# Kernel optimization log

Hardware: AMD Instinct MI355X
Metric: run time of the kernel (lower is better)

The kernel has to match this reference:

```python
import jax, jax.numpy as jnp
import numpy as np

D = 1024      # feat_dim
H = 16        # n_heads
HD = D // H   # head_dim
G = 32        # number of image/text groups
P = 128       # patch tokens per image
T = 32        # text tokens per caption
SUM_P = G * P # 4096
BT = G * T    # 1024


def setup_inputs() -> dict:
    key = jax.random.key(0)
    ks = jax.random.split(key, 16)
    s = (6.0 / (2 * D)) ** 0.5  # xavier_uniform bound
    def xavier(k):
        return jax.random.uniform(k, (D, D), jnp.float32, -s, s)
    return {
        "V_token": jax.random.normal(ks[0], (SUM_P, D), jnp.float32),
        "L_token": jax.random.normal(ks[1], (BT, D), jnp.float32),
        "image_split_list": jnp.full((G,), P, dtype=jnp.int32),
        "text_split_list": jnp.full((G,), T, dtype=jnp.int32),
        "Wq_w": xavier(ks[2]), "Wq_b": jnp.zeros((D,), jnp.float32),
        "Wk_w": xavier(ks[3]), "Wk_b": jnp.zeros((D,), jnp.float32),
        "Wv_w": xavier(ks[4]), "Wv_b": jnp.zeros((D,), jnp.float32),
        "Wo_w": xavier(ks[5]), "Wo_b": jnp.zeros((D,), jnp.float32),
        "Wm_w": xavier(ks[6]), "Wm_b": jnp.zeros((D,), jnp.float32),
        "Wv2_w": xavier(ks[7]), "Wv2_b": jnp.zeros((D,), jnp.float32),
    }


def reference(V_token, L_token, image_split_list, text_split_list,
              Wq_w, Wq_b, Wk_w, Wk_b, Wv_w, Wv_b,
              Wo_w, Wo_b, Wm_w, Wm_b, Wv2_w, Wv2_b):
    sum_p, bt = V_token.shape[0], L_token.shape[0]
    g = image_split_list.shape[0]
    # segment ids (equivalent to torch.cat of torch.full per group)
    v_seg = jnp.repeat(jnp.arange(g), image_split_list, total_repeat_length=sum_p)
    l_seg = jnp.repeat(jnp.arange(g), text_split_list, total_repeat_length=bt)
    mask = v_seg[:, None] != l_seg[None, :]  # [sum_p, bt], True = masked out

    Q = (V_token @ Wq_w.T + Wq_b).reshape(sum_p, H, HD)
    K = (L_token @ Wk_w.T + Wk_b).reshape(bt, H, HD)
    Vl = (L_token @ Wv_w.T + Wv_b).reshape(bt, H, HD)

    scores = jnp.einsum('phd,thd->hpt', Q, K) / (HD ** 0.5)  # [H, sum_p, bt]
    scores = jnp.where(mask[None, :, :], -jnp.inf, scores)
    attn = jax.nn.softmax(scores, axis=-1)
    ctx = jnp.einsum('hpt,thd->phd', attn, Vl).reshape(sum_p, D)

    out = ctx @ Wo_w.T + Wo_b
    mu = out @ Wm_w.T + Wm_b
    log_var = out @ Wv2_w.T + Wv2_b
    return mu, log_var, attn
```

## Files before the change

### kernel.cpp

```cpp
#include <hip/hip_runtime.h>
#include <hip/hip_fp16.h>

#define K_DIM 1024

typedef _Float16 f16x8 __attribute__((ext_vector_type(8)));
typedef _Float16 f16x4 __attribute__((ext_vector_type(4)));
typedef float f32x4_t __attribute__((ext_vector_type(4)));

__global__ __launch_bounds__(256) void cvt_f32_to_f16(const float* __restrict__ in,
                                                      _Float16* __restrict__ out, int n4) {
  int stride = gridDim.x * blockDim.x;
  for (int i = blockIdx.x * blockDim.x + threadIdx.x; i < n4; i += stride) {
    float4 v = reinterpret_cast<const float4*>(in)[i];
    f16x4 h;
    h[0] = (_Float16)v.x; h[1] = (_Float16)v.y; h[2] = (_Float16)v.z; h[3] = (_Float16)v.w;
    reinterpret_cast<f16x4*>(out)[i] = h;
  }
}

template <bool OUTH>
__global__ __launch_bounds__(256) void gemm_nt(
    const _Float16* __restrict__ A,
    const _Float16* __restrict__ Wa, const _Float16* __restrict__ Wb,
    const float* __restrict__ ba, const float* __restrict__ bb,
    void* __restrict__ Ca, void* __restrict__ Cb) {
  const _Float16* __restrict__ W = (blockIdx.z == 0) ? Wa : Wb;
  const float* __restrict__ bias = (blockIdx.z == 0) ? ba : bb;
  void* __restrict__ Cv = (blockIdx.z == 0) ? Ca : Cb;

  __shared__ _Float16 Ash[128][40];
  __shared__ _Float16 Bsh[128][40];

  const int tid = threadIdx.x;
  const int lane = tid & 63;
  const int wave = tid >> 6;
  const int wr = wave >> 1;
  const int wc = wave & 1;

  const int tm = blockIdx.x * 128;
  const int tn = blockIdx.y * 128;

  const int r0 = tid >> 2;
  const int kk0 = (tid & 3) * 8;

  const _Float16* Ag0 = A + (size_t)(tm + r0) * K_DIM + kk0;
  const _Float16* Ag1 = A + (size_t)(tm + r0 + 64) * K_DIM + kk0;
  const _Float16* Bg0 = W + (size_t)(tn + r0) * K_DIM + kk0;
  const _Float16* Bg1 = W + (size_t)(tn + r0 + 64) * K_DIM + kk0;

  f32x4_t acc[4][4];
#pragma unroll
  for (int m = 0; m < 4; ++m)
#pragma unroll
    for (int n = 0; n < 4; ++n) acc[m][n] = (f32x4_t){0.f, 0.f, 0.f, 0.f};

  uint4 pa0 = *(const uint4*)(Ag0);
  uint4 pa1 = *(const uint4*)(Ag1);
  uint4 pb0 = *(const uint4*)(Bg0);
  uint4 pb1 = *(const uint4*)(Bg1);

  const int fr = lane & 15;
  const int kc = (lane >> 4) * 8;

#pragma unroll 1
  for (int kt = 0; kt < K_DIM / 32; ++kt) {
    __syncthreads();
    *(uint4*)&Ash[r0][kk0] = pa0;
    *(uint4*)&Ash[r0 + 64][kk0] = pa1;
    *(uint4*)&Bsh[r0][kk0] = pb0;
    *(uint4*)&Bsh[r0 + 64][kk0] = pb1;
    __syncthreads();
    if (kt + 1 < K_DIM / 32) {
      const int koff = (kt + 1) * 32;
      pa0 = *(const uint4*)(Ag0 + koff);
      pa1 = *(const uint4*)(Ag1 + koff);
      pb0 = *(const uint4*)(Bg0 + koff);
      pb1 = *(const uint4*)(Bg1 + koff);
    }
    f16x8 af[4], bf[4];
#pragma unroll
    for (int m = 0; m < 4; ++m) af[m] = *(const f16x8*)&Ash[wr * 64 + m * 16 + fr][kc];
#pragma unroll
    for (int n = 0; n < 4; ++n) bf[n] = *(const f16x8*)&Bsh[wc * 64 + n * 16 + fr][kc];
#pragma unroll
    for (int m = 0; m < 4; ++m)
#pragma unroll
      for (int n = 0; n < 4; ++n)
        acc[m][n] = __builtin_amdgcn_mfma_f32_16x16x32_f16(af[m], bf[n], acc[m][n], 0, 0, 0);
  }

  const int cr = (lane >> 4) * 4;
  const int cc = lane & 15;
#pragma unroll
  for (int m = 0; m < 4; ++m) {
#pragma unroll
    for (int n = 0; n < 4; ++n) {
      const int col = tn + wc * 64 + n * 16 + cc;
      const float bv = bias[col];
#pragma unroll
      for (int r = 0; r < 4; ++r) {
        const int row = tm + wr * 64 + m * 16 + cr + r;
        float v = acc[m][n][r] + bv;
        if (OUTH)
          ((_Float16*)Cv)[(size_t)row * 1024 + col] = (_Float16)v;
        else
          ((float*)Cv)[(size_t)row * 1024 + col] = v;
      }
    }
  }
}

__global__ __launch_bounds__(256) void attn_kernel(
    const float* __restrict__ Q, const float* __restrict__ Kf, const float* __restrict__ Vf,
    float* __restrict__ attn_out,
    _Float16* __restrict__ ctx) {
  const int g = blockIdx.x;
  const int h = blockIdx.y;

  __shared__ float Ksh[32][68];
  __shared__ float Vsh[32][68];
  __shared__ float Arow[128][33];

  const int tid = threadIdx.x;

#pragma unroll
  for (int i = 0; i < 8; ++i) {
    int idx = tid + i * 256;
    int t = idx >> 6, d = idx & 63;
    Ksh[t][d] = Kf[(size_t)(g * 32 + t) * 1024 + h * 64 + d];
    Vsh[t][d] = Vf[(size_t)(g * 32 + t) * 1024 + h * 64 + d];
  }
  __syncthreads();

  const int p = tid >> 1;
  const int half = tid & 1;

  float4 qv[16];
  const float* qrow = Q + (size_t)(g * 128 + p) * 1024 + h * 64;
#pragma unroll
  for (int i = 0; i < 16; ++i) qv[i] = ((const float4*)qrow)[i];

  float s[16];
#pragma unroll
  for (int j = 0; j < 16; ++j) {
    int t = half * 16 + j;
    float acc = 0.f;
#pragma unroll
    for (int d4 = 0; d4 < 16; ++d4) {
      float4 kv = *(const float4*)&Ksh[t][d4 * 4];
      acc += qv[d4].x * kv.x + qv[d4].y * kv.y + qv[d4].z * kv.z + qv[d4].w * kv.w;
    }
    s[j] = acc * 0.125f;
  }

  float m = s[0];
#pragma unroll
  for (int j = 1; j < 16; ++j) m = fmaxf(m, s[j]);
  m = fmaxf(m, __shfl_xor(m, 1));
  float e[16];
  float sum = 0.f;
#pragma unroll
  for (int j = 0; j < 16; ++j) {
    e[j] = __expf(s[j] - m);
    sum += e[j];
  }
  sum += __shfl_xor(sum, 1);
  const float inv = 1.0f / sum;

  float* arow_out =
      attn_out + (size_t)h * 4096 * 1024 + (size_t)(g * 128 + p) * 1024 + g * 32 + half * 16;
#pragma unroll
  for (int j = 0; j < 16; ++j) {
    float a = e[j] * inv;
    arow_out[j] = a;
    Arow[p][half * 16 + j] = a;
  }
  __syncthreads();

  float4 acc4[8];
#pragma unroll
  for (int i = 0; i < 8; ++i) acc4[i] = (float4){0.f, 0.f, 0.f, 0.f};
#pragma unroll
  for (int t = 0; t < 32; ++t) {
    float av = Arow[p][t];
#pragma unroll
    for (int d4 = 0; d4 < 8; ++d4) {
      float4 v = *(const float4*)&Vsh[t][half * 32 + d4 * 4];
      acc4[d4].x += av * v.x;
      acc4[d4].y += av * v.y;
      acc4[d4].z += av * v.z;
      acc4[d4].w += av * v.w;
    }
  }
  _Float16* crow = ctx + (size_t)(g * 128 + p) * 1024 + h * 64 + half * 32;
#pragma unroll
  for (int i = 0; i < 4; ++i) {
    f16x8 hv;
    float4 lo = acc4[i * 2], hi = acc4[i * 2 + 1];
    hv[0] = (_Float16)lo.x; hv[1] = (_Float16)lo.y;
    hv[2] = (_Float16)lo.z; hv[3] = (_Float16)lo.w;
    hv[4] = (_Float16)hi.x; hv[5] = (_Float16)hi.y;
    hv[6] = (_Float16)hi.z; hv[7] = (_Float16)hi.w;
    *(f16x8*)&crow[i * 8] = hv;
  }
}

extern "C" void kernel_launch(void* const* d_in, const int* in_sizes, int n_in,
                              void* d_out, int out_size, void* d_ws, size_t ws_size,
                              hipStream_t stream) {
  const float* V_token = (const float*)d_in[0];
  const float* L_token = (const float*)d_in[1];
  const float* Wq_w = (const float*)d_in[4];
  const float* Wq_b = (const float*)d_in[5];
  const float* Wk_w = (const float*)d_in[6];
  const float* Wk_b = (const float*)d_in[7];
  const float* Wv_w = (const float*)d_in[8];
  const float* Wv_b = (const float*)d_in[9];
  const float* Wo_w = (const float*)d_in[10];
  const float* Wo_b = (const float*)d_in[11];
  const float* Wm_w = (const float*)d_in[12];
  const float* Wm_b = (const float*)d_in[13];
  const float* Wv2_w = (const float*)d_in[14];
  const float* Wv2_b = (const float*)d_in[15];

  char* ws = (char*)d_ws;
  _Float16* hV = (_Float16*)ws;  ws += (size_t)4096 * 1024 * 2;
  _Float16* hL = (_Float16*)ws;  ws += (size_t)1024 * 1024 * 2;
  _Float16* hWq = (_Float16*)ws; ws += (size_t)1024 * 1024 * 2;
  _Float16* hWk = (_Float16*)ws; ws += (size_t)1024 * 1024 * 2;
  _Float16* hWv = (_Float16*)ws; ws += (size_t)1024 * 1024 * 2;
  _Float16* hWo = (_Float16*)ws; ws += (size_t)1024 * 1024 * 2;
  _Float16* hWm = (_Float16*)ws; ws += (size_t)1024 * 1024 * 2;
  _Float16* hWv2 = (_Float16*)ws; ws += (size_t)1024 * 1024 * 2;
  float* Qf = (float*)ws;        ws += (size_t)4096 * 1024 * 4;
  float* Kf = (float*)ws;        ws += (size_t)1024 * 1024 * 4;
  float* Vf = (float*)ws;        ws += (size_t)1024 * 1024 * 4;
  _Float16* ctx = (_Float16*)ws; ws += (size_t)4096 * 1024 * 2;
  _Float16* outh = (_Float16*)ws; ws += (size_t)4096 * 1024 * 2;

  float* mu = (float*)d_out;
  float* logv = mu + (size_t)4096 * 1024;
  float* attn = mu + (size_t)2 * 4096 * 1024;

  hipMemsetAsync(attn, 0, (size_t)16 * 4096 * 1024 * 4, stream);

  auto cvt = [&](const float* in, _Float16* out, size_t n) {
    int n4 = (int)(n / 4);
    int blocks = (n4 + 255) / 256;
    if (blocks > 2048) blocks = 2048;
    hipLaunchKernelGGL(cvt_f32_to_f16, dim3(blocks), dim3(256), 0, stream, in, out, n4);
  };
  cvt(V_token, hV, (size_t)4096 * 1024);
  cvt(L_token, hL, (size_t)1024 * 1024);
  cvt(Wq_w, hWq, (size_t)1024 * 1024);
  cvt(Wk_w, hWk, (size_t)1024 * 1024);
  cvt(Wv_w, hWv, (size_t)1024 * 1024);
  cvt(Wo_w, hWo, (size_t)1024 * 1024);
  cvt(Wm_w, hWm, (size_t)1024 * 1024);
  cvt(Wv2_w, hWv2, (size_t)1024 * 1024);

  hipLaunchKernelGGL((gemm_nt<false>), dim3(32, 8, 1), dim3(256), 0, stream,
                     hV, hWq, hWq, Wq_b, Wq_b, (void*)Qf, (void*)Qf);
  hipLaunchKernelGGL((gemm_nt<false>), dim3(8, 8, 2), dim3(256), 0, stream,
                     hL, hWk, hWv, Wk_b, Wv_b, (void*)Kf, (void*)Vf);
  hipLaunchKernelGGL(attn_kernel, dim3(32, 16), dim3(256), 0, stream, Qf, Kf, Vf, attn, ctx);
  hipLaunchKernelGGL((gemm_nt<true>), dim3(32, 8, 1), dim3(256), 0, stream,
                     ctx, hWo, hWo, Wo_b, Wo_b, (void*)outh, (void*)outh);
  hipLaunchKernelGGL((gemm_nt<false>), dim3(32, 8, 2), dim3(256), 0, stream,
                     outh, hWm, hWv2, Wm_b, Wv2_b, (void*)mu, (void*)logv);
}
```

Measured before the change: 176.8 us.

## Fuse attn zero-fill into GEMM launches and shrink GEMM tiles to 128x64

Drops the standalone memset of the large attention output and splits the zero-fill across two GEMM kernels as extra z-slices. Heads 0-7 are zeroed alongside the QKV projection. Off-diagonal blocks of heads 8-15 are zeroed alongside the mu/logvar projection, skipping the blocks the attention kernel writes. It also batches the eight fp32-to-fp16 conversions into one launch, merges the Q/K/V GEMMs into one launch, and halves the GEMM N-tile to 64 for more blocks. The intent is to overlap the memory-bound fill with compute and cut launch count, at the cost of less reuse per GEMM tile and uneven block workloads.

```diff
diff --git a/kernel.cpp b/kernel.cpp
--- a/kernel.cpp
+++ b/kernel.cpp
@@ -1,35 +1,37 @@
 #include <hip/hip_runtime.h>
 #include <hip/hip_fp16.h>
-
-#define K_DIM 1024
 
 typedef _Float16 f16x8 __attribute__((ext_vector_type(8)));
 typedef _Float16 f16x4 __attribute__((ext_vector_type(4)));
 typedef float f32x4_t __attribute__((ext_vector_type(4)));
 
-__global__ __launch_bounds__(256) void cvt_f32_to_f16(const float* __restrict__ in,
-                                                      _Float16* __restrict__ out, int n4) {
-  int stride = gridDim.x * blockDim.x;
+struct CvtArgs {
+  const float* src[8];
+  _Float16* dst[8];
+  int n4[8];
+};
+
+__global__ __launch_bounds__(256) void cvt_all(CvtArgs a) {
+  const int t = blockIdx.y;
+  const float4* __restrict__ in = (const float4*)a.src[t];
+  f16x4* __restrict__ out = (f16x4*)a.dst[t];
+  const int n4 = a.n4[t];
+  const int stride = gridDim.x * blockDim.x;
   for (int i = blockIdx.x * blockDim.x + threadIdx.x; i < n4; i += stride) {
-    float4 v = reinterpret_cast<const float4*>(in)[i];
+    float4 v = in[i];
     f16x4 h;
     h[0] = (_Float16)v.x; h[1] = (_Float16)v.y; h[2] = (_Float16)v.z; h[3] = (_Float16)v.w;
-    reinterpret_cast<f16x4*>(out)[i] = h;
+    out[i] = h;
   }
 }
 
 template <bool OUTH>
-__global__ __launch_bounds__(256) void gemm_nt(
-    const _Float16* __restrict__ A,
-    const _Float16* __restrict__ Wa, const _Float16* __restrict__ Wb,
-    const float* __restrict__ ba, const float* __restrict__ bb,
-    void* __restrict__ Ca, void* __restrict__ Cb) {
-  const _Float16* __restrict__ W = (blockIdx.z == 0) ? Wa : Wb;
-  const float* __restrict__ bias = (blockIdx.z == 0) ? ba : bb;
-  void* __restrict__ Cv = (blockIdx.z == 0) ? Ca : Cb;
-
+__device__ __forceinline__ void gemm_tile(const _Float16* __restrict__ A,
+                                          const _Float16* __restrict__ W,
+                                          const float* __restrict__ bias,
+                                          void* __restrict__ Cv, int tm, int tn) {
   __shared__ _Float16 Ash[128][40];
-  __shared__ _Float16 Bsh[128][40];
+  __shared__ _Float16 Bsh[64][40];
 
   const int tid = threadIdx.x;
   const int lane = tid & 63;
@@ -37,55 +39,49 @@
   const int wr = wave >> 1;
   const int wc = wave & 1;
 
-  const int tm = blockIdx.x * 128;
-  const int tn = blockIdx.y * 128;
-
-  const int r0 = tid >> 2;
-  const int kk0 = (tid & 3) * 8;
-
-  const _Float16* Ag0 = A + (size_t)(tm + r0) * K_DIM + kk0;
-  const _Float16* Ag1 = A + (size_t)(tm + r0 + 64) * K_DIM + kk0;
-  const _Float16* Bg0 = W + (size_t)(tn + r0) * K_DIM + kk0;
-  const _Float16* Bg1 = W + (size_t)(tn + r0 + 64) * K_DIM + kk0;
-
-  f32x4_t acc[4][4];
+  const int ar = tid >> 1;
+  const int ac = (tid & 1) * 16;
+  const int br = tid >> 2;
+  const int bc = (tid & 3) * 8;
+
+  const _Float16* Ag = A + (size_t)(tm + ar) * 1024 + ac;
+  const _Float16* Bg = W + (size_t)(tn + br) * 1024 + bc;
+
+  f32x4_t acc[4][2];
 #pragma unroll
   for (int m = 0; m < 4; ++m)
 #pragma unroll
-    for (int n = 0; n < 4; ++n) acc[m][n] = (f32x4_t){0.f, 0.f, 0.f, 0.f};
-
-  uint4 pa0 = *(const uint4*)(Ag0);
-  uint4 pa1 = *(const uint4*)(Ag1);
-  uint4 pb0 = *(const uint4*)(Bg0);
-  uint4 pb1 = *(const uint4*)(Bg1);
+    for (int n = 0; n < 2; ++n) acc[m][n] = (f32x4_t){0.f, 0.f, 0.f, 0.f};
+
+  uint4 pa0 = *(const uint4*)(Ag);
+  uint4 pa1 = *(const uint4*)(Ag + 8);
+  uint4 pb = *(const uint4*)(Bg);
 
   const int fr = lane & 15;
   const int kc = (lane >> 4) * 8;
 
 #pragma unroll 1
-  for (int kt = 0; kt < K_DIM / 32; ++kt) {
+  for (int kt = 0; kt < 32; ++kt) {
     __syncthreads();
-    *(uint4*)&Ash[r0][kk0] = pa0;
-    *(uint4*)&Ash[r0 + 64][kk0] = pa1;
-    *(uint4*)&Bsh[r0][kk0] = pb0;
-    *(uint4*)&Bsh[r0 + 64][kk0] = pb1;
+    *(uint4*)&Ash[ar][ac] = pa0;
+    *(uint4*)&Ash[ar][ac + 8] = pa1;
+    *(uint4*)&Bsh[br][bc] = pb;
     __syncthreads();
-    if (kt + 1 < K_DIM / 32) {
-      const int koff = (kt + 1) * 32;
-      pa0 = *(const uint4*)(Ag0 + koff);
-      pa1 = *(const uint4*)(Ag1 + koff);
-      pb0 = *(const uint4*)(Bg0 + koff);
-      pb1 = *(const uint4*)(Bg1 + koff);
-    }
-    f16x8 af[4], bf[4];
+    if (kt + 1 < 32) {
+      const int ko = (kt + 1) * 32;
+      pa0 = *(const uint4*)(Ag + ko);
+      pa1 = *(const uint4*)(Ag + ko + 8);
+      pb = *(const uint4*)(Bg + ko);
+    }
+    f16x8 af[4], bf[2];
 #pragma unroll
     for (int m = 0; m < 4; ++m) af[m] = *(const f16x8*)&Ash[wr * 64 + m * 16 + fr][kc];
 #pragma unroll
-    for (int n = 0; n < 4; ++n) bf[n] = *(const f16x8*)&Bsh[wc * 64 + n * 16 + fr][kc];
+    for (int n = 0; n < 2; ++n) bf[n] = *(const f16x8*)&Bsh[wc * 32 + n * 16 + fr][kc];
 #pragma unroll
     for (int m = 0; m < 4; ++m)
 #pragma unroll
-      for (int n = 0; n < 4; ++n)
+      for (int n = 0; n < 2; ++n)
         acc[m][n] = __builtin_amdgcn_mfma_f32_16x16x32_f16(af[m], bf[n], acc[m][n], 0, 0, 0);
   }
 
@@ -94,8 +90,8 @@
 #pragma unroll
   for (int m = 0; m < 4; ++m) {
 #pragma unroll
-    for (int n = 0; n < 4; ++n) {
-      const int col = tn + wc * 64 + n * 16 + cc;
+    for (int n = 0; n < 2; ++n) {
+      const int col = tn + wc * 32 + n * 16 + cc;
       const float bv = bias[col];
 #pragma unroll
       for (int r = 0; r < 4; ++r) {
@@ -108,6 +104,67 @@
       }
     }
   }
+}
+
+__global__ __launch_bounds__(256) void gemm_qkv_fill(
+    const _Float16* __restrict__ hV, const _Float16* __restrict__ hL,
+    const _Float16* __restrict__ hWq, const _Float16* __restrict__ hWk,
+    const _Float16* __restrict__ hWv,
+    const float* __restrict__ bq, const float* __restrict__ bk, const float* __restrict__ bv,
+    float* __restrict__ Qf, float* __restrict__ Kf, float* __restrict__ Vf,
+    float* __restrict__ attn) {
+  const int z = blockIdx.z;
+  if (z == 3) {
+    const int bl = blockIdx.y * 32 + blockIdx.x;
+    float4* base = (float4*)attn + (size_t)bl * 16384;
+    const float4 z4 = {0.f, 0.f, 0.f, 0.f};
+#pragma unroll
+    for (int c = threadIdx.x; c < 16384; c += 256) base[c] = z4;
+    return;
+  }
+  if (z != 0 && blockIdx.x >= 8) return;
+
+  const _Float16* A = (z == 0) ? hV : hL;
+  const _Float16* W = (z == 0) ? hWq : (z == 1) ? hWk : hWv;
+  const float* bias = (z == 0) ? bq : (z == 1) ? bk : bv;
+  float* C = (z == 0) ? Qf : (z == 1) ? Kf : Vf;
+  gemm_tile<false>(A, W, bias, (void*)C, blockIdx.x * 128, blockIdx.y * 64);
+}
+
+__global__ __launch_bounds__(256) void gemm_wo(
+    const _Float16* __restrict__ ctx, const _Float16* __restrict__ hWo,
+    const float* __restrict__ bo, _Float16* __restrict__ outh) {
+  gemm_tile<true>(ctx, hWo, bo, (void*)outh, blockIdx.x * 128, blockIdx.y * 64);
+}
+
+__global__ __launch_bounds__(256) void gemm_mv_fill(
+    const _Float16* __restrict__ outh,
+    const _Float16* __restrict__ hWm, const _Float16* __restrict__ hWv2,
+    const float* __restrict__ bm, const float* __restrict__ bv2,
+    float* __restrict__ mu, float* __restrict__ logv, float* __restrict__ attn) {
+  const int z = blockIdx.z;
+  if (z == 2) {
+    const int bl = blockIdx.y * 32 + blockIdx.x;
+    const int wave = threadIdx.x >> 6;
+    const int lane = threadIdx.x & 63;
+    const float4 z4 = {0.f, 0.f, 0.f, 0.f};
+#pragma unroll
+    for (int i = 0; i < 16; ++i) {
+      const int rowIdx = bl * 64 + i * 4 + wave;
+      const int p = rowIdx & 4095;
+      const int g8 = (p >> 7) * 8;
+      float4* row = (float4*)(attn + ((size_t)(8 + (rowIdx >> 12)) * 4096 + p) * 1024);
+#pragma unroll
+      for (int c = lane; c < 256; c += 64) {
+        if (c < g8 || c >= g8 + 8) row[c] = z4;
+      }
+    }
+    return;
+  }
+  const _Float16* W = z ? hWv2 : hWm;
+  const float* bias = z ? bv2 : bm;
+  float* C = z ? logv : mu;
+  gemm_tile<false>(outh, W, bias, (void*)C, blockIdx.x * 128, blockIdx.y * 64);
 }
 
 __global__ __launch_bounds__(256) void attn_kernel(
@@ -224,48 +281,42 @@
   const float* Wv2_b = (const float*)d_in[15];
 
   char* ws = (char*)d_ws;
-  _Float16* hV = (_Float16*)ws;  ws += (size_t)4096 * 1024 * 2;
-  _Float16* hL = (_Float16*)ws;  ws += (size_t)1024 * 1024 * 2;
-  _Float16* hWq = (_Float16*)ws; ws += (size_t)1024 * 1024 * 2;
-  _Float16* hWk = (_Float16*)ws; ws += (size_t)1024 * 1024 * 2;
-  _Float16* hWv = (_Float16*)ws; ws += (size_t)1024 * 1024 * 2;
-  _Float16* hWo = (_Float16*)ws; ws += (size_t)1024 * 1024 * 2;
-  _Float16* hWm = (_Float16*)ws; ws += (size_t)1024 * 1024 * 2;
+  _Float16* hV = (_Float16*)ws;   ws += (size_t)4096 * 1024 * 2;
+  _Float16* hL = (_Float16*)ws;   ws += (size_t)1024 * 1024 * 2;
+  _Float16* hWq = (_Float16*)ws;  ws += (size_t)1024 * 1024 * 2;
+  _Float16* hWk = (_Float16*)ws;  ws += (size_t)1024 * 1024 * 2;
+  _Float16* hWv = (_Float16*)ws;  ws += (size_t)1024 * 1024 * 2;
+  _Float16* hWo = (_Float16*)ws;  ws += (size_t)1024 * 1024 * 2;
+  _Float16* hWm = (_Float16*)ws;  ws += (size_t)1024 * 1024 * 2;
   _Float16* hWv2 = (_Float16*)ws; ws += (size_t)1024 * 1024 * 2;
-  float* Qf = (float*)ws;        ws += (size_t)4096 * 1024 * 4;
-  float* Kf = (float*)ws;        ws += (size_t)1024 * 1024 * 4;
-  float* Vf = (float*)ws;        ws += (size_t)1024 * 1024 * 4;
-  _Float16* ctx = (_Float16*)ws; ws += (size_t)4096 * 1024 * 2;
+  float* Qf = (float*)ws;         ws += (size_t)4096 * 1024 * 4;
+  float* Kf = (float*)ws;         ws += (size_t)1024 * 1024 * 4;
+  float* Vf = (float*)ws;         ws += (size_t)1024 * 1024 * 4;
+  _Float16* ctx = (_Float16*)ws;  ws += (size_t)4096 * 1024 * 2;
   _Float16* outh = (_Float16*)ws; ws += (size_t)4096 * 1024 * 2;
 
   float* mu = (float*)d_out;
   float* logv = mu + (size_t)4096 * 1024;
   float* attn = mu + (size_t)2 * 4096 * 1024;
 
-  hipMemsetAsync(attn, 0, (size_t)16 * 4096 * 1024 * 4, stream);
-
-  auto cvt = [&](const float* in, _Float16* out, size_t n) {
-    int n4 = (int)(n / 4);
-    int blocks = (n4 + 255) / 256;
-    if (blocks > 2048) blocks = 2048;
-    hipLaunchKernelGGL(cvt_f32_to_f16, dim3(blocks), dim3(256), 0, stream, in, out, n4);
-  };
-  cvt(V_token, hV, (size_t)4096 * 1024);
-  cvt(L_token, hL, (size_t)1024 * 1024);
-  cvt(Wq_w, hWq, (size_t)1024 * 1024);
-  cvt(Wk_w, hWk, (size_t)1024 * 1024);
-  cvt(Wv_w, hWv, (size_t)1024 * 1024);
-  cvt(Wo_w, hWo, (size_t)1024 * 1024);
-  cvt(Wm_w, hWm, (size_t)1024 * 1024);
-  cvt(Wv2_w, hWv2, (size_t)1024 * 1024);
-
-  hipLaunchKernelGGL((gemm_nt<false>), dim3(32, 8, 1), dim3(256), 0, stream,
-                     hV, hWq, hWq, Wq_b, Wq_b, (void*)Qf, (void*)Qf);
-  hipLaunchKernelGGL((gemm_nt<false>), dim3(8, 8, 2), dim3(256), 0, stream,
-                     hL, hWk, hWv, Wk_b, Wv_b, (void*)Kf, (void*)Vf);
+  CvtArgs ca;
+  ca.src[0] = V_token; ca.dst[0] = hV;  ca.n4[0] = 4096 * 1024 / 4;
+  ca.src[1] = L_token; ca.dst[1] = hL;  ca.n4[1] = 1024 * 1024 / 4;
+  ca.src[2] = Wq_w;  ca.dst[2] = hWq;  ca.n4[2] = 1024 * 1024 / 4;
+  ca.src[3] = Wk_w;  ca.dst[3] = hWk;  ca.n4[3] = 1024 * 1024 / 4;
+  ca.src[4] = Wv_w;  ca.dst[4] = hWv;  ca.n4[4] = 1024 * 1024 / 4;
+  ca.src[5] = Wo_w;  ca.dst[5] = hWo;  ca.n4[5] = 1024 * 1024 / 4;
+  ca.src[6] = Wm_w;  ca.dst[6] = hWm;  ca.n4[6] = 1024 * 1024 / 4;
+  ca.src[7] = Wv2_w; ca.dst[7] = hWv2; ca.n4[7] = 1024 * 1024 / 4;
+  hipLaunchKernelGGL(cvt_all, dim3(128, 8), dim3(256), 0, stream, ca);
+
+  hipLaunchKernelGGL(gemm_qkv_fill, dim3(32, 16, 4), dim3(256), 0, stream,
+                     hV, hL, hWq, hWk, hWv, Wq_b, Wk_b, Wv_b, Qf, Kf, Vf, attn);
+
   hipLaunchKernelGGL(attn_kernel, dim3(32, 16), dim3(256), 0, stream, Qf, Kf, Vf, attn, ctx);
-  hipLaunchKernelGGL((gemm_nt<true>), dim3(32, 8, 1), dim3(256), 0, stream,
-                     ctx, hWo, hWo, Wo_b, Wo_b, (void*)outh, (void*)outh);
-  hipLaunchKernelGGL((gemm_nt<false>), dim3(32, 8, 2), dim3(256), 0, stream,
-                     outh, hWm, hWv2, Wm_b, Wv2_b, (void*)mu, (void*)logv);
-}
+
+  hipLaunchKernelGGL(gemm_wo, dim3(32, 16), dim3(256), 0, stream, ctx, hWo, Wo_b, outh);
+
+  hipLaunchKernelGGL(gemm_mv_fill, dim3(32, 16, 3), dim3(256), 0, stream,
+                     outh, hWm, hWv2, Wm_b, Wv2_b, mu, logv, attn);
+}
```

Measured after the change: 175.5 us. No clear change (-0.7%).
